# Kernel tuning notes

Hardware: AMD Instinct MI355X
Metric: run time of the kernel (lower is better)

## Reference

```python
import jax, jax.numpy as jnp
import numpy as np

N_NODES = 50000
N_EDGES = 800000
HIDDEN = 128
OUT = 128


def setup_inputs() -> dict:
    key = jax.random.key(0)
    k1, k2, k3, k4, k5, k6 = jax.random.split(key, 6)
    h = jax.random.normal(k1, (N_NODES, HIDDEN), dtype=jnp.float32)
    src = jax.random.randint(k2, (N_EDGES,), 0, N_NODES, dtype=jnp.int64)
    dst = jax.random.randint(k3, (N_EDGES,), 0, N_NODES, dtype=jnp.int64)
    scale = 1.0 / np.sqrt(HIDDEN)
    W_edge = jax.random.normal(k4, (OUT, HIDDEN), dtype=jnp.float32) * scale
    W_self = jax.random.normal(k5, (OUT, HIDDEN), dtype=jnp.float32) * scale
    b_self = jax.random.normal(k6, (OUT,), dtype=jnp.float32) * scale
    return {"h": h, "src": src, "dst": dst, "W_edge": W_edge, "W_self": W_self, "b_self": b_self}


def reference(h, src, dst, W_edge, W_self, b_self):
    n = h.shape[0]
    # edge_transform(src_features): same linear on every edge -> transform nodes once, then gather
    msg_node = h @ W_edge.T                       # [N, OUT]
    msg = msg_node[src]                           # [E, OUT] gather
    sums = jax.ops.segment_sum(msg, dst, num_segments=n)  # [N, OUT] scatter-add
    deg = jax.ops.segment_sum(jnp.ones((dst.shape[0],), dtype=h.dtype), dst, num_segments=n)
    h1 = sums / jnp.maximum(deg, 1.0)[:, None]    # mean; zero in-degree -> 0 (DGL semantics)
    out = jax.nn.relu(h @ W_self.T + b_self + h1)
    return out
```

## Files before the change

kernel.cpp:

```cpp
#include <hip/hip_runtime.h>

#define N_HID 128
#define CAP   64
#define OVF_CAP 8192
#define NSLICE 8
#define PBLK   256
#define LDW   132

typedef short bf16x8 __attribute__((ext_vector_type(8)));
typedef float f32x4  __attribute__((ext_vector_type(4)));

static __device__ __forceinline__ unsigned short f2bf(float f)
{
    unsigned int u = __float_as_uint(f);
    u = (u + 0x7fffu + ((u >> 16) & 1u)) >> 16;
    return (unsigned short)u;
}
static __device__ __forceinline__ unsigned int pack2(float a, float b)
{
    return (unsigned int)f2bf(a) | ((unsigned int)f2bf(b) << 16);
}
static __device__ __forceinline__ float bf2f(unsigned int bits16)
{
    return __uint_as_float(bits16 << 16);
}
static __device__ __forceinline__ int slice_of(int d, float sln)
{
    int sl = (int)((float)d * sln);
    return sl > NSLICE - 1 ? NSLICE - 1 : sl;
}

__global__ __launch_bounds__(256) void count_fragw(
    const int* __restrict__ dst, int* __restrict__ blockCnt,
    int* __restrict__ cnt, int* __restrict__ ovfn, int E, int n, float sln,
    const float* __restrict__ We, const float* __restrict__ Ws,
    unsigned short* __restrict__ Be, unsigned short* __restrict__ Bs)
{
    int t = threadIdx.x, b = blockIdx.x;

    if (b >= PBLK) {
        int bb = b - PBLK;
        const float* srcw = (bb < 8) ? We : Ws;
        unsigned short* dstF = (bb < 8) ? Be : Bs;
        int rt = bb & 7;
        int kc = t >> 6, l = t & 63, m = l & 15, q = l >> 4;
        const float* p = &srcw[(size_t)(rt * 16 + m) * N_HID + kc * 32 + q * 8];
        float4 v0 = *(const float4*)p;
        float4 v1 = *(const float4*)(p + 4);
        uint4 pk;
        pk.x = pack2(v0.x, v0.y);
        pk.y = pack2(v0.z, v0.w);
        pk.z = pack2(v1.x, v1.y);
        pk.w = pack2(v1.z, v1.w);
        *(uint4*)&dstF[(size_t)rt * 2048 + kc * 512 + l * 8] = pk;
        return;
    }

    for (int i = b * 256 + t; i < n; i += PBLK * 256) cnt[i] = 0;
    if (b == 0 && t == 0) *ovfn = 0;

    int c[NSLICE];
#pragma unroll
    for (int s = 0; s < NSLICE; ++s) c[s] = 0;

    for (int e = b * 256 + t; e < E; e += PBLK * 256) {
        int sl = slice_of(dst[e], sln);
#pragma unroll
        for (int s = 0; s < NSLICE; ++s) c[s] += (sl == s);
    }

    __shared__ int red[NSLICE * 4];
    int lane = t & 63, wid = t >> 6;
#pragma unroll
    for (int s = 0; s < NSLICE; ++s) {
        int v = c[s];
#pragma unroll
        for (int off = 32; off; off >>= 1) v += __shfl_down(v, off);
        if (lane == 0) red[s * 4 + wid] = v;
    }
    __syncthreads();
    if (t < NSLICE)
        blockCnt[t * PBLK + b] = red[t*4+0] + red[t*4+1] + red[t*4+2] + red[t*4+3];
}

__global__ __launch_bounds__(256) void scan_gemm(
    const int* __restrict__ blockCnt, int* __restrict__ blockBase,
    int* __restrict__ sbase, int E,
    const float* __restrict__ h,
    const unsigned short* __restrict__ Be,
    const unsigned short* __restrict__ Bsf,
    const float* __restrict__ bias,
    unsigned short* __restrict__ msgOut,
    float* __restrict__ fOut,
    int n, int nrt)
{
    __shared__ float As[4][16 * LDW];

    int t = threadIdx.x;
    if (blockIdx.x == 0) {
        __shared__ int wsm[4];
        int lane = t & 63, wid = t >> 6;
        int v[8]; int s = 0;
#pragma unroll
        for (int i = 0; i < 8; ++i) { v[i] = blockCnt[t * 8 + i]; s += v[i]; }
        int val = s;
#pragma unroll
        for (int off = 1; off < 64; off <<= 1) {
            int y = __shfl_up(val, off);
            if (lane >= off) val += y;
        }
        if (lane == 63) wsm[wid] = val;
        __syncthreads();
        if (t == 0) { int a = 0; for (int w = 0; w < 4; ++w) { int tmp = wsm[w]; wsm[w] = a; a += tmp; } }
        __syncthreads();
        int excl = wsm[wid] + val - s;
#pragma unroll
        for (int i = 0; i < 8; ++i) { int tv = v[i]; blockBase[t * 8 + i] = excl; excl += tv; }
        __syncthreads();
        if (t < NSLICE) sbase[t] = blockBase[t * PBLK];
        if (t == 0)     sbase[NSLICE] = E;
        return;
    }

    int w = t >> 6, l = t & 63;
    int rt = (blockIdx.x - 1) * 4 + w;
    bool active = rt < nrt;
    int rtc = active ? rt : nrt - 1;
    int row0 = rtc * 16;

    float* A = As[w];
#pragma unroll
    for (int it = 0; it < 8; ++it) {
        int f  = it * 64 + l;
        int r  = f >> 5;
        int c4 = (f & 31) * 4;
        int gr = row0 + r; if (gr > n - 1) gr = n - 1;
        *(float4*)&A[r * LDW + c4] = *(const float4*)&h[(size_t)gr * N_HID + c4];
    }
    __syncthreads();

    int m = l & 15, q = l >> 4;
    union { uint4 u; bf16x8 v; } af[4];
#pragma unroll
    for (int kc = 0; kc < 4; ++kc) {
        const float* p = &A[m * LDW + kc * 32 + q * 8];
        float4 v0 = *(const float4*)p;
        float4 v1 = *(const float4*)(p + 4);
        af[kc].u.x = pack2(v0.x, v0.y);
        af[kc].u.y = pack2(v0.z, v0.w);
        af[kc].u.z = pack2(v1.x, v1.y);
        af[kc].u.w = pack2(v1.z, v1.w);
    }

    const int colb = l & 15;
    const int rq   = (l >> 4) * 4;

#pragma unroll 1
    for (int pass = 0; pass < 2; ++pass) {
        const unsigned short* Bfrag = pass ? Bsf : Be;
#pragma unroll
        for (int ct = 0; ct < 8; ++ct) {
            const bf16x8* Bp = (const bf16x8*)(Bfrag + (size_t)ct * 2048);
            f32x4 acc = {0.f, 0.f, 0.f, 0.f};
            acc = __builtin_amdgcn_mfma_f32_16x16x32_bf16(af[0].v, Bp[l],       acc, 0, 0, 0);
            acc = __builtin_amdgcn_mfma_f32_16x16x32_bf16(af[1].v, Bp[64 + l],  acc, 0, 0, 0);
            acc = __builtin_amdgcn_mfma_f32_16x16x32_bf16(af[2].v, Bp[128 + l], acc, 0, 0, 0);
            acc = __builtin_amdgcn_mfma_f32_16x16x32_bf16(af[3].v, Bp[192 + l], acc, 0, 0, 0);

            if (active) {
                int col = ct * 16 + colb;
                if (pass) {
                    float bv = bias[col];
#pragma unroll
                    for (int r = 0; r < 4; ++r) {
                        int row = row0 + rq + r;
                        if (row < n) fOut[(size_t)row * N_HID + col] = acc[r] + bv;
                    }
                } else {
#pragma unroll
                    for (int r = 0; r < 4; ++r) {
                        int row = row0 + rq + r;
                        if (row < n) msgOut[(size_t)row * N_HID + col] = f2bf(acc[r]);
                    }
                }
            }
        }
    }
}

__global__ __launch_bounds__(256) void part_scatter(
    const int* __restrict__ src, const int* __restrict__ dst,
    const int* __restrict__ blockBase, unsigned int* __restrict__ part,
    int E, int n, float sln)
{
    __shared__ int cur[NSLICE];
    int t = threadIdx.x, b = blockIdx.x;
    if (t < NSLICE) cur[t] = blockBase[t * PBLK + b];
    __syncthreads();
    for (int e = b * 256 + t; e < E; e += PBLK * 256) {
        int d = dst[e], s = src[e];
        int sl  = slice_of(d, sln);
        int pos = atomicAdd(&cur[sl], 1);
        part[pos] = ((unsigned int)d << 16) | (unsigned int)s;
    }
}

__global__ __launch_bounds__(256) void bucket_scatter2(
    const unsigned int* __restrict__ part,
    const int* __restrict__ sbase,
    int* __restrict__ cnt,
    unsigned short* __restrict__ bucket,
    int* __restrict__ ovfn,
    long long* __restrict__ ovf)
{
    const int slice = blockIdx.x & 7;
    const int g     = blockIdx.x >> 3;
    const int nG    = (int)(gridDim.x >> 3);
    const int lo    = sbase[slice];
    const int hi    = sbase[slice + 1];
    const int m     = hi - lo;

    const int chunk = (m + nG - 1) / nG;
    const int e0 = lo + g * chunk;
    int e1 = e0 + chunk; if (e1 > hi) e1 = hi;

    for (int e = e0 + (int)threadIdx.x; e < e1; e += 256) {
        unsigned int pk = part[e];
        int d = (int)(pk >> 16);
        int s = (int)(pk & 0xffffu);
        int c = atomicAdd(&cnt[d], 1);
        if (c < CAP) {
            bucket[(size_t)d * CAP + c] = (unsigned short)s;
        } else {
            int o = atomicAdd(ovfn, 1);
            if (o < OVF_CAP) ovf[o] = ((long long)d << 32) | (unsigned int)s;
        }
    }
}

__global__ __launch_bounds__(256) void gather_finish(
    const int* __restrict__ cnt,
    const unsigned short* __restrict__ bucket,
    const int* __restrict__ ovfn,
    const long long* __restrict__ ovf,
    const unsigned short* __restrict__ msg,
    float* __restrict__ out,
    int n)
{
    int node = blockIdx.x * 4 + (threadIdx.x >> 6);
    if (node >= n) return;
    int lane = threadIdx.x & 63;
    int deg  = cnt[node];
    int m    = deg < CAP ? deg : CAP;

    const unsigned short* bk = &bucket[(size_t)node * CAP];
    const unsigned int* m32 = (const unsigned int*)msg;

    float ax = 0.f, ay = 0.f;
    int i = 0;
    for (; i + 4 <= m; i += 4) {
        ushort4 ss = *(const ushort4*)&bk[i];
        unsigned int v0 = m32[(size_t)ss.x * 64 + lane];
        unsigned int v1 = m32[(size_t)ss.y * 64 + lane];
        unsigned int v2 = m32[(size_t)ss.z * 64 + lane];
        unsigned int v3 = m32[(size_t)ss.w * 64 + lane];
        ax += bf2f(v0 & 0xffffu) + bf2f(v1 & 0xffffu) + bf2f(v2 & 0xffffu) + bf2f(v3 & 0xffffu);
        ay += bf2f(v0 >> 16)     + bf2f(v1 >> 16)     + bf2f(v2 >> 16)     + bf2f(v3 >> 16);
    }
    for (; i < m; ++i) {
        unsigned int v = m32[(size_t)bk[i] * 64 + lane];
        ax += bf2f(v & 0xffffu);
        ay += bf2f(v >> 16);
    }

    if (deg > CAP) {
        int no = *ovfn; if (no > OVF_CAP) no = OVF_CAP;
        for (int o = 0; o < no; ++o) {
            long long pk = ovf[o];
            if ((int)(pk >> 32) == node) {
                unsigned int v = m32[(size_t)(unsigned int)pk * 64 + lane];
                ax += bf2f(v & 0xffffu);
                ay += bf2f(v >> 16);
            }
        }
    }

    float sc = deg > 0 ? 1.0f / (float)deg : 0.f;

    float2* o2 = (float2*)out;
    float2 sv  = o2[(size_t)node * 64 + lane];
    float2 r;
    r.x = fmaxf(sv.x + ax * sc, 0.f);
    r.y = fmaxf(sv.y + ay * sc, 0.f);
    o2[(size_t)node * 64 + lane] = r;
}

extern "C" void kernel_launch(void* const* d_in, const int* in_sizes, int n_in,
                              void* d_out, int out_size, void* d_ws, size_t ws_size,
                              hipStream_t stream)
{
    const float* h   = (const float*)d_in[0];
    const int*   src = (const int*)d_in[1];
    const int*   dst = (const int*)d_in[2];
    const float* We  = (const float*)d_in[3];
    const float* Ws  = (const float*)d_in[4];
    const float* bs  = (const float*)d_in[5];
    float*       out = (float*)d_out;

    const int n   = in_sizes[0] / N_HID;
    const int E   = in_sizes[1];
    const int nrt = (n + 15) / 16;
    const float sln = (float)NSLICE / (float)n;

    unsigned short* msg = (unsigned short*)d_ws;
    unsigned short* bucket = msg + (size_t)n * N_HID;
    unsigned short* Be  = bucket + (size_t)n * CAP;
    unsigned short* Bs  = Be + 8 * 2048;
    int*  cnt  = (int*)(Bs + 8 * 2048);
    int*  ovfn = cnt + n;
    long long* ovf = (long long*)(ovfn + 8);
    int*  blockCnt  = (int*)(ovf + OVF_CAP);
    int*  blockBase = blockCnt + PBLK * NSLICE;
    int*  sbase     = blockBase + PBLK * NSLICE;
    unsigned int* part = (unsigned int*)(sbase + 16);

    count_fragw<<<PBLK + 16, 256, 0, stream>>>(dst, blockCnt, cnt, ovfn, E, n, sln,
                                               We, Ws, Be, Bs);
    scan_gemm<<<1 + (nrt + 3) / 4, 256, 0, stream>>>(blockCnt, blockBase, sbase, E,
                                                     h, Be, Bs, bs, msg, out, n, nrt);
    part_scatter<<<PBLK, 256, 0, stream>>>(src, dst, blockBase, part, E, n, sln);
    bucket_scatter2<<<1024, 256, 0, stream>>>(part, sbase, cnt, bucket, ovfn, ovf);
    gather_finish<<<(n + 3) / 4, 256, 0, stream>>>(cnt, bucket, ovfn, ovf, msg, out, n);
}
```

Baseline: 189.4 us.

## Aggregate raw features before edge transform and fuse both GEMMs after gather

Reorders the computation to take the mean of bf16-cast node features over neighbors first, then apply W_edge. The aggregated rows are written straight into the MFMA fragment layout, and a final kernel runs the self and edge GEMMs together with bias and ReLU. This drops the fp32 output round-trip between the GEMM and gather stages and the separate msg buffer. In exchange it adds a cast pass and an extra kernel, and the mean is now rounded to bf16 before the GEMM. The bucket CAP is also halved, so more high-degree nodes will fall back to the slow overflow path.

New measurement: 189.0 us. About the same (-0.2%).

```diff
diff --git a/kernel.cpp b/kernel.cpp
--- a/kernel.cpp
+++ b/kernel.cpp
@@ -1,11 +1,10 @@
 #include <hip/hip_runtime.h>
 
 #define N_HID 128
-#define CAP   64
+#define CAP   32
 #define OVF_CAP 8192
 #define NSLICE 8
 #define PBLK   256
-#define LDW   132
 
 typedef short bf16x8 __attribute__((ext_vector_type(8)));
 typedef float f32x4  __attribute__((ext_vector_type(4)));
@@ -83,19 +82,11 @@
         blockCnt[t * PBLK + b] = red[t*4+0] + red[t*4+1] + red[t*4+2] + red[t*4+3];
 }
 
-__global__ __launch_bounds__(256) void scan_gemm(
+__global__ __launch_bounds__(256) void scan_cast(
     const int* __restrict__ blockCnt, int* __restrict__ blockBase,
     int* __restrict__ sbase, int E,
-    const float* __restrict__ h,
-    const unsigned short* __restrict__ Be,
-    const unsigned short* __restrict__ Bsf,
-    const float* __restrict__ bias,
-    unsigned short* __restrict__ msgOut,
-    float* __restrict__ fOut,
-    int n, int nrt)
-{
-    __shared__ float As[4][16 * LDW];
-
+    const float* __restrict__ h, unsigned short* __restrict__ hbf, int total)
+{
     int t = threadIdx.x;
     if (blockIdx.x == 0) {
         __shared__ int wsm[4];
@@ -121,70 +112,16 @@
         if (t == 0)     sbase[NSLICE] = E;
         return;
     }
-
-    int w = t >> 6, l = t & 63;
-    int rt = (blockIdx.x - 1) * 4 + w;
-    bool active = rt < nrt;
-    int rtc = active ? rt : nrt - 1;
-    int row0 = rtc * 16;
-
-    float* A = As[w];
-#pragma unroll
-    for (int it = 0; it < 8; ++it) {
-        int f  = it * 64 + l;
-        int r  = f >> 5;
-        int c4 = (f & 31) * 4;
-        int gr = row0 + r; if (gr > n - 1) gr = n - 1;
-        *(float4*)&A[r * LDW + c4] = *(const float4*)&h[(size_t)gr * N_HID + c4];
-    }
-    __syncthreads();
-
-    int m = l & 15, q = l >> 4;
-    union { uint4 u; bf16x8 v; } af[4];
-#pragma unroll
-    for (int kc = 0; kc < 4; ++kc) {
-        const float* p = &A[m * LDW + kc * 32 + q * 8];
-        float4 v0 = *(const float4*)p;
-        float4 v1 = *(const float4*)(p + 4);
-        af[kc].u.x = pack2(v0.x, v0.y);
-        af[kc].u.y = pack2(v0.z, v0.w);
-        af[kc].u.z = pack2(v1.x, v1.y);
-        af[kc].u.w = pack2(v1.z, v1.w);
-    }
-
-    const int colb = l & 15;
-    const int rq   = (l >> 4) * 4;
-
-#pragma unroll 1
-    for (int pass = 0; pass < 2; ++pass) {
-        const unsigned short* Bfrag = pass ? Bsf : Be;
-#pragma unroll
-        for (int ct = 0; ct < 8; ++ct) {
-            const bf16x8* Bp = (const bf16x8*)(Bfrag + (size_t)ct * 2048);
-            f32x4 acc = {0.f, 0.f, 0.f, 0.f};
-            acc = __builtin_amdgcn_mfma_f32_16x16x32_bf16(af[0].v, Bp[l],       acc, 0, 0, 0);
-            acc = __builtin_amdgcn_mfma_f32_16x16x32_bf16(af[1].v, Bp[64 + l],  acc, 0, 0, 0);
-            acc = __builtin_amdgcn_mfma_f32_16x16x32_bf16(af[2].v, Bp[128 + l], acc, 0, 0, 0);
-            acc = __builtin_amdgcn_mfma_f32_16x16x32_bf16(af[3].v, Bp[192 + l], acc, 0, 0, 0);
-
-            if (active) {
-                int col = ct * 16 + colb;
-                if (pass) {
-                    float bv = bias[col];
-#pragma unroll
-                    for (int r = 0; r < 4; ++r) {
-                        int row = row0 + rq + r;
-                        if (row < n) fOut[(size_t)row * N_HID + col] = acc[r] + bv;
-                    }
-                } else {
-#pragma unroll
-                    for (int r = 0; r < 4; ++r) {
-                        int row = row0 + rq + r;
-                        if (row < n) msgOut[(size_t)row * N_HID + col] = f2bf(acc[r]);
-                    }
-                }
-            }
-        }
+    int idx = ((int)blockIdx.x - 1) * 2048 + t * 8;
+    if (idx + 8 <= total) {
+        float4 v0 = *(const float4*)&h[idx];
+        float4 v1 = *(const float4*)&h[idx + 4];
+        uint4 pk;
+        pk.x = pack2(v0.x, v0.y);
+        pk.y = pack2(v0.z, v0.w);
+        pk.z = pack2(v1.x, v1.y);
+        pk.w = pack2(v1.z, v1.w);
+        *(uint4*)&hbf[idx] = pk;
     }
 }
 
@@ -238,13 +175,13 @@
     }
 }
 
-__global__ __launch_bounds__(256) void gather_finish(
+__global__ __launch_bounds__(256) void gather_mean(
     const int* __restrict__ cnt,
     const unsigned short* __restrict__ bucket,
     const int* __restrict__ ovfn,
     const long long* __restrict__ ovf,
-    const unsigned short* __restrict__ msg,
-    float* __restrict__ out,
+    const unsigned short* __restrict__ hbf,
+    unsigned short* __restrict__ hagg,
     int n)
 {
     int node = blockIdx.x * 4 + (threadIdx.x >> 6);
@@ -254,21 +191,21 @@
     int m    = deg < CAP ? deg : CAP;
 
     const unsigned short* bk = &bucket[(size_t)node * CAP];
-    const unsigned int* m32 = (const unsigned int*)msg;
+    const unsigned int* h32 = (const unsigned int*)hbf;
 
     float ax = 0.f, ay = 0.f;
     int i = 0;
     for (; i + 4 <= m; i += 4) {
         ushort4 ss = *(const ushort4*)&bk[i];
-        unsigned int v0 = m32[(size_t)ss.x * 64 + lane];
-        unsigned int v1 = m32[(size_t)ss.y * 64 + lane];
-        unsigned int v2 = m32[(size_t)ss.z * 64 + lane];
-        unsigned int v3 = m32[(size_t)ss.w * 64 + lane];
+        unsigned int v0 = h32[(size_t)ss.x * 64 + lane];
+        unsigned int v1 = h32[(size_t)ss.y * 64 + lane];
+        unsigned int v2 = h32[(size_t)ss.z * 64 + lane];
+        unsigned int v3 = h32[(size_t)ss.w * 64 + lane];
         ax += bf2f(v0 & 0xffffu) + bf2f(v1 & 0xffffu) + bf2f(v2 & 0xffffu) + bf2f(v3 & 0xffffu);
         ay += bf2f(v0 >> 16)     + bf2f(v1 >> 16)     + bf2f(v2 >> 16)     + bf2f(v3 >> 16);
     }
     for (; i < m; ++i) {
-        unsigned int v = m32[(size_t)bk[i] * 64 + lane];
+        unsigned int v = h32[(size_t)bk[i] * 64 + lane];
         ax += bf2f(v & 0xffffu);
         ay += bf2f(v >> 16);
     }
@@ -278,7 +215,7 @@
         for (int o = 0; o < no; ++o) {
             long long pk = ovf[o];
             if ((int)(pk >> 32) == node) {
-                unsigned int v = m32[(size_t)(unsigned int)pk * 64 + lane];
+                unsigned int v = h32[(size_t)(unsigned int)pk * 64 + lane];
                 ax += bf2f(v & 0xffffu);
                 ay += bf2f(v >> 16);
             }
@@ -287,12 +224,61 @@
 
     float sc = deg > 0 ? 1.0f / (float)deg : 0.f;
 
-    float2* o2 = (float2*)out;
-    float2 sv  = o2[(size_t)node * 64 + lane];
-    float2 r;
-    r.x = fmaxf(sv.x + ax * sc, 0.f);
-    r.y = fmaxf(sv.y + ay * sc, 0.f);
-    o2[(size_t)node * 64 + lane] = r;
+    int rt = node >> 4, mm = node & 15;
+    int kc = lane >> 4, q = (lane >> 2) & 3, j = (lane & 3) * 2;
+    unsigned int pk = pack2(ax * sc, ay * sc);
+    *(unsigned int*)&hagg[(size_t)rt * 2048 + kc * 512 + (q * 16 + mm) * 8 + j] = pk;
+}
+
+__global__ __launch_bounds__(256) void gemm_final(
+    const unsigned short* __restrict__ hbf,
+    const unsigned short* __restrict__ hagg,
+    const unsigned short* __restrict__ Be,
+    const unsigned short* __restrict__ Bsf,
+    const float* __restrict__ bias,
+    float* __restrict__ out,
+    int n, int nrt)
+{
+    int w = (int)((blockIdx.x * blockDim.x + threadIdx.x) >> 6);
+    if (w >= nrt) return;
+    int l = threadIdx.x & 63;
+    int m = l & 15, q = l >> 4;
+    int row0 = w * 16;
+
+    bf16x8 ah[4];
+#pragma unroll
+    for (int kc = 0; kc < 4; ++kc) {
+        int gr = row0 + m; if (gr > n - 1) gr = n - 1;
+        ah[kc] = *(const bf16x8*)&hbf[(size_t)gr * N_HID + kc * 32 + q * 8];
+    }
+    const bf16x8* Gp = (const bf16x8*)(hagg + (size_t)w * 2048);
+    bf16x8 ag0 = Gp[l], ag1 = Gp[64 + l], ag2 = Gp[128 + l], ag3 = Gp[192 + l];
+
+    const int colb = l & 15;
+    const int rq   = (l >> 4) * 4;
+
+#pragma unroll
+    for (int ct = 0; ct < 8; ++ct) {
+        const bf16x8* BpS = (const bf16x8*)(Bsf + (size_t)ct * 2048);
+        const bf16x8* BpE = (const bf16x8*)(Be  + (size_t)ct * 2048);
+        f32x4 acc = {0.f, 0.f, 0.f, 0.f};
+        acc = __builtin_amdgcn_mfma_f32_16x16x32_bf16(ah[0], BpS[l],       acc, 0, 0, 0);
+        acc = __builtin_amdgcn_mfma_f32_16x16x32_bf16(ah[1], BpS[64 + l],  acc, 0, 0, 0);
+        acc = __builtin_amdgcn_mfma_f32_16x16x32_bf16(ah[2], BpS[128 + l], acc, 0, 0, 0);
+        acc = __builtin_amdgcn_mfma_f32_16x16x32_bf16(ah[3], BpS[192 + l], acc, 0, 0, 0);
+        acc = __builtin_amdgcn_mfma_f32_16x16x32_bf16(ag0,   BpE[l],       acc, 0, 0, 0);
+        acc = __builtin_amdgcn_mfma_f32_16x16x32_bf16(ag1,   BpE[64 + l],  acc, 0, 0, 0);
+        acc = __builtin_amdgcn_mfma_f32_16x16x32_bf16(ag2,   BpE[128 + l], acc, 0, 0, 0);
+        acc = __builtin_amdgcn_mfma_f32_16x16x32_bf16(ag3,   BpE[192 + l], acc, 0, 0, 0);
+
+        int col = ct * 16 + colb;
+        float bv = bias[col];
+#pragma unroll
+        for (int r = 0; r < 4; ++r) {
+            int row = row0 + rq + r;
+            if (row < n) out[(size_t)row * N_HID + col] = fmaxf(acc[r] + bv, 0.f);
+        }
+    }
 }
 
 extern "C" void kernel_launch(void* const* d_in, const int* in_sizes, int n_in,
@@ -311,9 +297,11 @@
     const int E   = in_sizes[1];
     const int nrt = (n + 15) / 16;
     const float sln = (float)NSLICE / (float)n;
-
-    unsigned short* msg = (unsigned short*)d_ws;
-    unsigned short* bucket = msg + (size_t)n * N_HID;
+    const int total = n * N_HID;
+
+    unsigned short* hbf  = (unsigned short*)d_ws;
+    unsigned short* hagg = hbf + (size_t)n * N_HID;
+    unsigned short* bucket = hagg + (size_t)nrt * 2048;
     unsigned short* Be  = bucket + (size_t)n * CAP;
     unsigned short* Bs  = Be + 8 * 2048;
     int*  cnt  = (int*)(Bs + 8 * 2048);
@@ -324,11 +312,14 @@
     int*  sbase     = blockBase + PBLK * NSLICE;
     unsigned int* part = (unsigned int*)(sbase + 16);
 
+    const int castBlocks = (total + 2047) / 2048;
+
     count_fragw<<<PBLK + 16, 256, 0, stream>>>(dst, blockCnt, cnt, ovfn, E, n, sln,
                                                We, Ws, Be, Bs);
-    scan_gemm<<<1 + (nrt + 3) / 4, 256, 0, stream>>>(blockCnt, blockBase, sbase, E,
-                                                     h, Be, Bs, bs, msg, out, n, nrt);
+    scan_cast<<<1 + castBlocks, 256, 0, stream>>>(blockCnt, blockBase, sbase, E,
+                                                  h, hbf, total);
     part_scatter<<<PBLK, 256, 0, stream>>>(src, dst, blockBase, part, E, n, sln);
     bucket_scatter2<<<1024, 256, 0, stream>>>(part, sbase, cnt, bucket, ovfn, ovf);
-    gather_finish<<<(n + 3) / 4, 256, 0, stream>>>(cnt, bucket, ovfn, ovf, msg, out, n);
-}
+    gather_mean<<<(n + 3) / 4, 256, 0, stream>>>(cnt, bucket, ovfn, ovf, hbf, hagg, n);
+    gemm_final<<<(nrt + 3) / 4, 256, 0, stream>>>(hbf, hagg, Be, Bs, bs, out, n, nrt);
+}
```
